# Performance work log

Hardware: AMD Instinct MI355X
Metric: run time of the kernel (lower is better)

## Reference

```python
import jax, jax.numpy as jnp
import numpy as np
import math

B, S, D = 1, 4096, 2048
H, KVH, HD = 32, 8, 64
W = 512            # sliding window size (== block size)
THETA = 10000.0
EPS = 1e-5
INTER = 5632
PRE_SCALE = 1.0 / math.sqrt(2.0)


def setup_inputs() -> dict:
    key = jax.random.key(0)
    ks = jax.random.split(key, 8)
    def w(k, shape, fan_in):
        return jax.random.normal(k, shape, jnp.float32) * (fan_in ** -0.5)
    return {
        "hidden_states": jax.random.normal(ks[0], (B, S, D), jnp.float32),
        "mixer_norm_w": jnp.ones((D,), jnp.float32),
        "wq": w(ks[1], (D, H * HD), D),
        "wk": w(ks[2], (D, KVH * HD), D),
        "wv": w(ks[3], (D, KVH * HD), D),
        "wo": w(ks[4], (H * HD, D), H * HD),
        "mlp_norm_w": jnp.ones((D,), jnp.float32),
        "w_gate": w(ks[5], (D, 2 * INTER), D),
        "w_down": w(ks[6], (INTER, D), INTER),
    }


def rmsnorm(x, w, eps=EPS):
    return x * jax.lax.rsqrt(jnp.mean(x * x, axis=-1, keepdims=True) + eps) * w


def rope(x):
    # x: [B, S, h, HD]; rotate-half RoPE
    half = HD // 2
    inv_freq = 1.0 / (THETA ** (jnp.arange(0, HD, 2, dtype=jnp.float32) / HD))
    freqs = jnp.arange(S, dtype=jnp.float32)[:, None] * inv_freq[None, :]  # [S, half]
    cos = jnp.cos(freqs)[None, :, None, :]
    sin = jnp.sin(freqs)[None, :, None, :]
    x1, x2 = x[..., :half], x[..., half:]
    return jnp.concatenate([x1 * cos - x2 * sin, x2 * cos + x1 * sin], axis=-1)


def sliding_attention(x, wq, wk, wv, wo):
    # x already pre-scaled; returns attn output (pre /pre_scale)
    q = (x @ wq).reshape(B, S, H, HD)
    k = (x @ wk).reshape(B, S, KVH, HD)
    v = (x @ wv).reshape(B, S, KVH, HD)
    q, k = rope(q), rope(k)
    rep = H // KVH
    k = jnp.repeat(k, rep, axis=2)  # [B,S,H,HD]
    v = jnp.repeat(v, rep, axis=2)
    nb = S // W
    qb = q.reshape(B, nb, W, H, HD)
    kb = k.reshape(B, nb, W, H, HD)
    vb = v.reshape(B, nb, W, H, HD)
    zeros = jnp.zeros((B, 1, W, H, HD), q.dtype)
    kw = jnp.concatenate([jnp.concatenate([zeros, kb[:, :-1]], axis=1), kb], axis=2)  # [B,nb,2W,H,HD]
    vw = jnp.concatenate([jnp.concatenate([zeros, vb[:, :-1]], axis=1), vb], axis=2)
    # local mask [nb, W, 2W]
    blk = jnp.arange(nb)[:, None, None]
    q_pos = blk * W + jnp.arange(W)[None, :, None]
    k_pos = blk * W - W + jnp.arange(2 * W)[None, None, :]
    mask = (k_pos >= 0) & (k_pos <= q_pos) & (q_pos - k_pos < W)
    scores = jnp.einsum("bnqhd,bnkhd->bhnqk", qb, kw) * (HD ** -0.5)
    scores = jnp.where(mask[None, None], scores, jnp.finfo(scores.dtype).min)
    p = jax.nn.softmax(scores, axis=-1)
    out = jnp.einsum("bhnqk,bnkhd->bnqhd", p, vw).reshape(B, S, H * HD)
    return out @ wo


def reference(hidden_states, mixer_norm_w, wq, wk, wv, wo, mlp_norm_w, w_gate, w_down):
    residual = hidden_states
    x = rmsnorm(hidden_states, mixer_norm_w)
    attn_out = sliding_attention(x * PRE_SCALE, wq, wk, wv, wo) / PRE_SCALE
    h = residual + attn_out
    xn = rmsnorm(h, mlp_norm_w)
    gv = xn @ w_gate
    gate, y = gv[..., :INTER], gv[..., INTER:]
    mlp_out = (jax.nn.silu(gate) * y) @ w_down
    return h + mlp_out
```

## Files before the change

kernel.cpp:

```cpp
#include <hip/hip_runtime.h>
#include <stdint.h>

typedef __attribute__((ext_vector_type(8))) short s16x8;
typedef __attribute__((ext_vector_type(4))) float f32x4;

#define GLD_LDS16(gp, lp) __builtin_amdgcn_global_load_lds( \
    (__attribute__((address_space(1))) void*)(void*)(gp), \
    (__attribute__((address_space(3))) void*)(lp), 16, 0, 0)

__device__ __forceinline__ float b2f(unsigned short s) {
    unsigned int u = ((unsigned int)s) << 16;
    return __builtin_bit_cast(float, u);
}
__device__ __forceinline__ unsigned short f2b(float f) {
    unsigned int u = __builtin_bit_cast(unsigned int, f);
    u = (u + 0x7FFFu + ((u >> 16) & 1u)) >> 16;
    return (unsigned short)u;
}
__device__ __forceinline__ f32x4 mfma16(s16x8 a, s16x8 b, f32x4 c) {
    return __builtin_amdgcn_mfma_f32_16x16x32_bf16(a, b, c, 0, 0, 0);
}
template <int N> __device__ __forceinline__ void waitvm() {
    if constexpr (N == 3) asm volatile("s_waitcnt vmcnt(3)" ::: "memory");
    else if constexpr (N == 4) asm volatile("s_waitcnt vmcnt(4)" ::: "memory");
    else if constexpr (N == 6) asm volatile("s_waitcnt vmcnt(6)" ::: "memory");
}

__global__ __launch_bounds__(256) void rmsnorm_bf16(
    const float* __restrict__ x, const float* __restrict__ wgt,
    unsigned short* __restrict__ out)
{
    const int row = blockIdx.x;
    const int t = threadIdx.x;
    const float* xr = x + (size_t)row * 2048;
    float4 a = *(const float4*)(xr + t * 8);
    float4 b = *(const float4*)(xr + t * 8 + 4);
    float ss = a.x*a.x + a.y*a.y + a.z*a.z + a.w*a.w
             + b.x*b.x + b.y*b.y + b.z*b.z + b.w*b.w;
    #pragma unroll
    for (int d = 1; d < 64; d <<= 1) ss += __shfl_xor(ss, d);
    __shared__ float red[4];
    if ((t & 63) == 0) red[t >> 6] = ss;
    __syncthreads();
    float tot = red[0] + red[1] + red[2] + red[3];
    float inv = rsqrtf(tot * (1.0f / 2048.0f) + 1e-5f);
    float vals[8] = {a.x, a.y, a.z, a.w, b.x, b.y, b.z, b.w};
    const float* wr_ = wgt + t * 8;
    s16x8 ov;
    #pragma unroll
    for (int j = 0; j < 8; ++j) ov[j] = (short)f2b(vals[j] * inv * wr_[j]);
    *(s16x8*)(out + (size_t)row * 2048 + t * 8) = ov;
}

__global__ __launch_bounds__(256) void transpose_to_bf16(
    const float* __restrict__ in, unsigned short* __restrict__ out, int K, int N)
{
    __shared__ float tile[32][33];
    int n0 = blockIdx.x * 32, k0 = blockIdx.y * 32;
    int r = threadIdx.x >> 5, c = threadIdx.x & 31;
    #pragma unroll
    for (int i = 0; i < 4; ++i)
        tile[r + i * 8][c] = in[(size_t)(k0 + r + i * 8) * N + n0 + c];
    __syncthreads();
    #pragma unroll
    for (int i = 0; i < 4; ++i)
        out[(size_t)(n0 + r + i * 8) * K + k0 + c] = f2b(tile[c][r + i * 8]);
}

template <int BN, int EPI>
__global__ __launch_bounds__(512, 2) void gemmq(
    const unsigned short* __restrict__ A,
    const unsigned short* __restrict__ B,
    void* __restrict__ Cv,
    const float* __restrict__ ADD,
    int N, int K)
{
    constexpr int WN  = BN / 4;
    constexpr int HN  = WN / 2;
    constexpr int NJQ = WN / 32;
    constexpr int NBU = BN / 64;
    constexpr int ABUF = 256 * 64;
    constexpr int BBUF = BN * 64;
    constexpr int W_P0 = 4;
    constexpr int W_P1 = (BN == 256) ? 6 : 4;
    constexpr int W_P2 = (BN == 256) ? 4 : 3;
    __shared__ __align__(16) unsigned short As[2 * ABUF];
    __shared__ __align__(16) unsigned short Bs[2 * BBUF];

    const int t = threadIdx.x;
    const int l = t & 63, w = t >> 6;
    const int l15 = l & 15, lg = l >> 4;
    const int wr = w >> 2, wc = w & 3;
    const int x7 = l15 & 7;
    const int cc0 = ((lg) ^ x7) << 3;
    const int cc1 = ((4 | lg) ^ x7) << 3;

    const int nwg = (int)gridDim.x;
    const int orig = (int)blockIdx.x;
    const int q8 = nwg >> 3, r8 = nwg & 7;
    const int xcd = orig & 7, lid = orig >> 3;
    const int wg = (xcd < r8 ? xcd * (q8 + 1) : r8 * (q8 + 1) + (xcd - r8) * q8) + lid;
    const int m0 = (wg & 15) * 256;
    const int n0 = (wg >> 4) * BN;

    const int tr = t >> 3;
    const int scol = ((t & 7) ^ (tr & 7)) << 3;
    const unsigned short* pA[4];
    #pragma unroll
    for (int u = 0; u < 4; ++u) {
        const int lrow = u * 64 + tr;
        const int g = ((lrow >> 6) & 1) * 128 + (lrow >> 7) * 64 + (lrow & 63);
        pA[u] = A + (size_t)(m0 + g) * K + scol;
    }
    const unsigned short* pB[NBU];
    #pragma unroll
    for (int u = 0; u < NBU; ++u) {
        const int lrow = u * 64 + tr;
        const int h = lrow / (BN / 2), rem = lrow % (BN / 2);
        const int g = (rem / HN) * WN + h * HN + (rem % HN);
        pB[u] = B + (size_t)(n0 + g) * K + scol;
    }

    f32x4 acc[2][2][4][NJQ] = {};
    s16x8 aF[4][2];
    s16x8 bF[2][NJQ][2];

    const int NT = K / 64;

    GLD_LDS16(pA[0], &As[0 * 4096 + t * 8]);
    GLD_LDS16(pA[1], &As[1 * 4096 + t * 8]);
    #pragma unroll
    for (int u = 0; u < NBU; ++u) GLD_LDS16(pB[u], &Bs[u * 4096 + t * 8]);
    GLD_LDS16(pA[2], &As[2 * 4096 + t * 8]);
    GLD_LDS16(pA[3], &As[3 * 4096 + t * 8]);
    waitvm<W_P2>();
    __builtin_amdgcn_s_barrier();

    for (int kt = 0; kt < NT; ++kt) {
        const int rb  = (kt & 1) ? ABUF : 0;
        const int rbB = (kt & 1) ? BBUF : 0;
        const int wb  = ABUF - rb;
        const int wbB = BBUF - rbB;
        const int knext = (kt + 1 < NT ? kt + 1 : kt) * 64;

        #pragma unroll
        for (int i = 0; i < 4; ++i) {
            const int lr = wr * 64 + i * 16 + l15;
            aF[i][0] = *(const s16x8*)&As[rb + lr * 64 + cc0];
            aF[i][1] = *(const s16x8*)&As[rb + lr * 64 + cc1];
        }
        #pragma unroll
        for (int j = 0; j < NJQ; ++j) {
            const int lr = wc * HN + j * 16 + l15;
            bF[0][j][0] = *(const s16x8*)&Bs[rbB + lr * 64 + cc0];
            bF[0][j][1] = *(const s16x8*)&Bs[rbB + lr * 64 + cc1];
        }
        GLD_LDS16(pA[0] + knext, &As[wb + 0 * 4096 + t * 8]);
        GLD_LDS16(pA[1] + knext, &As[wb + 1 * 4096 + t * 8]);
        __builtin_amdgcn_s_barrier();
        __builtin_amdgcn_s_setprio(1);
        #pragma unroll
        for (int kk = 0; kk < 2; ++kk)
            #pragma unroll
            for (int i = 0; i < 4; ++i)
                #pragma unroll
                for (int j = 0; j < NJQ; ++j)
                    acc[0][0][i][j] = mfma16(aF[i][kk], bF[0][j][kk], acc[0][0][i][j]);
        __builtin_amdgcn_s_setprio(0);
        waitvm<W_P0>();
        __builtin_amdgcn_s_barrier();

        #pragma unroll
        for (int j = 0; j < NJQ; ++j) {
            const int lr = (BN / 2) + wc * HN + j * 16 + l15;
            bF[1][j][0] = *(const s16x8*)&Bs[rbB + lr * 64 + cc0];
            bF[1][j][1] = *(const s16x8*)&Bs[rbB + lr * 64 + cc1];
        }
        #pragma unroll
        for (int u = 0; u < NBU; ++u)
            GLD_LDS16(pB[u] + knext, &Bs[wbB + u * 4096 + t * 8]);
        __builtin_amdgcn_s_barrier();
        __builtin_amdgcn_s_setprio(1);
        #pragma unroll
        for (int kk = 0; kk < 2; ++kk)
            #pragma unroll
            for (int i = 0; i < 4; ++i)
                #pragma unroll
                for (int j = 0; j < NJQ; ++j)
                    acc[0][1][i][j] = mfma16(aF[i][kk], bF[1][j][kk], acc[0][1][i][j]);
        __builtin_amdgcn_s_setprio(0);
        waitvm<W_P1>();
        __builtin_amdgcn_s_barrier();

        #pragma unroll
        for (int i = 0; i < 4; ++i) {
            const int lr = 128 + wr * 64 + i * 16 + l15;
            aF[i][0] = *(const s16x8*)&As[rb + lr * 64 + cc0];
            aF[i][1] = *(const s16x8*)&As[rb + lr * 64 + cc1];
        }
        GLD_LDS16(pA[2] + knext, &As[wb + 2 * 4096 + t * 8]);
        GLD_LDS16(pA[3] + knext, &As[wb + 3 * 4096 + t * 8]);
        __builtin_amdgcn_s_barrier();
        __builtin_amdgcn_s_setprio(1);
        #pragma unroll
        for (int kk = 0; kk < 2; ++kk)
            #pragma unroll
            for (int i = 0; i < 4; ++i)
                #pragma unroll
                for (int j = 0; j < NJQ; ++j)
                    acc[1][0][i][j] = mfma16(aF[i][kk], bF[0][j][kk], acc[1][0][i][j]);
        #pragma unroll
        for (int kk = 0; kk < 2; ++kk)
            #pragma unroll
            for (int i = 0; i < 4; ++i)
                #pragma unroll
                for (int j = 0; j < NJQ; ++j)
                    acc[1][1][i][j] = mfma16(aF[i][kk], bF[1][j][kk], acc[1][1][i][j]);
        __builtin_amdgcn_s_setprio(0);
        waitvm<W_P2>();
        __builtin_amdgcn_s_barrier();
    }

    #pragma unroll
    for (int qm = 0; qm < 2; ++qm)
        #pragma unroll
        for (int i = 0; i < 4; ++i)
            #pragma unroll
            for (int r = 0; r < 4; ++r) {
                const int row = m0 + wr * 128 + qm * 64 + i * 16 + lg * 4 + r;
                const size_t rbase = (size_t)row * N;
                #pragma unroll
                for (int qn = 0; qn < 2; ++qn)
                    #pragma unroll
                    for (int j = 0; j < NJQ; ++j) {
                        const int col = n0 + wc * WN + qn * HN + j * 16 + l15;
                        float v = acc[qm][qn][i][j][r];
                        if constexpr (EPI == 0) {
                            ((unsigned short*)Cv)[rbase + col] = f2b(v);
                        } else {
                            ((float*)Cv)[rbase + col] = v + ADD[rbase + col];
                        }
                    }
            }
}

__global__ __launch_bounds__(512, 2) void gemm_glu(
    const unsigned short* __restrict__ A,
    const unsigned short* __restrict__ Bg,
    const unsigned short* __restrict__ By,
    unsigned short* __restrict__ act,
    int N, int K)
{
    constexpr int ABUF = 256 * 64, BBUF = 128 * 64;
    __shared__ __align__(16) unsigned short As[2 * ABUF];
    __shared__ __align__(16) unsigned short Bgs[2 * BBUF];
    __shared__ __align__(16) unsigned short Bys[2 * BBUF];

    const int t = threadIdx.x;
    const int l = t & 63, w = t >> 6;
    const int l15 = l & 15, lg = l >> 4;
    const int wr = w >> 2, wc = w & 3;
    const int x7 = l15 & 7;
    const int cc0 = ((lg) ^ x7) << 3;
    const int cc1 = ((4 | lg) ^ x7) << 3;

    const int nwg = (int)gridDim.x;
    const int orig = (int)blockIdx.x;
    const int q8 = nwg >> 3;
    const int xcd = orig & 7, lid = orig >> 3;
    const int wg = xcd * q8 + lid;
    const int m0 = (wg & 15) * 256;
    const int n0 = (wg >> 4) * 128;

    const int tr = t >> 3;
    const int scol = ((t & 7) ^ (tr & 7)) << 3;
    const unsigned short* pA[4];
    #pragma unroll
    for (int u = 0; u < 4; ++u) {
        const int lrow = u * 64 + tr;
        const int g = ((lrow >> 6) & 1) * 128 + (lrow >> 7) * 64 + (lrow & 63);
        pA[u] = A + (size_t)(m0 + g) * K + scol;
    }
    const unsigned short *pG[2], *pY[2];
    #pragma unroll
    for (int u = 0; u < 2; ++u) {
        const int g = (tr >> 4) * 32 + u * 16 + (tr & 15);
        pG[u] = Bg + (size_t)(n0 + g) * K + scol;
        pY[u] = By + (size_t)(n0 + g) * K + scol;
    }

    f32x4 accG[2][2][4] = {};
    f32x4 accY[2][2][4] = {};
    s16x8 aF[4][2];
    s16x8 gF[2][2], yF[2][2];

    const int NT = K / 64;

    GLD_LDS16(pA[0], &As[0 * 4096 + t * 8]);
    GLD_LDS16(pA[1], &As[1 * 4096 + t * 8]);
    GLD_LDS16(pG[0], &Bgs[0 * 4096 + t * 8]);
    GLD_LDS16(pY[0], &Bys[0 * 4096 + t * 8]);
    GLD_LDS16(pG[1], &Bgs[1 * 4096 + t * 8]);
    GLD_LDS16(pY[1], &Bys[1 * 4096 + t * 8]);
    GLD_LDS16(pA[2], &As[2 * 4096 + t * 8]);
    GLD_LDS16(pA[3], &As[3 * 4096 + t * 8]);
    waitvm<4>();
    __builtin_amdgcn_s_barrier();

    for (int kt = 0; kt < NT; ++kt) {
        const int rb  = (kt & 1) ? ABUF : 0;
        const int rbB = (kt & 1) ? BBUF : 0;
        const int wb  = ABUF - rb;
        const int wbB = BBUF - rbB;
        const int knext = (kt + 1 < NT ? kt + 1 : kt) * 64;

        #pragma unroll
        for (int i = 0; i < 4; ++i) {
            const int lr = wr * 64 + i * 16 + l15;
            aF[i][0] = *(const s16x8*)&As[rb + lr * 64 + cc0];
            aF[i][1] = *(const s16x8*)&As[rb + lr * 64 + cc1];
        }
        {
            const int lr = wc * 16 + l15;
            gF[0][0] = *(const s16x8*)&Bgs[rbB + lr * 64 + cc0];
            gF[0][1] = *(const s16x8*)&Bgs[rbB + lr * 64 + cc1];
            yF[0][0] = *(const s16x8*)&Bys[rbB + lr * 64 + cc0];
            yF[0][1] = *(const s16x8*)&Bys[rbB + lr * 64 + cc1];
        }
        GLD_LDS16(pA[0] + knext, &As[wb + 0 * 4096 + t * 8]);
        GLD_LDS16(pA[1] + knext, &As[wb + 1 * 4096 + t * 8]);
        __builtin_amdgcn_s_barrier();
        __builtin_amdgcn_s_setprio(1);
        #pragma unroll
        for (int kk = 0; kk < 2; ++kk)
            #pragma unroll
            for (int i = 0; i < 4; ++i) {
                accG[0][0][i] = mfma16(aF[i][kk], gF[0][kk], accG[0][0][i]);
                accY[0][0][i] = mfma16(aF[i][kk], yF[0][kk], accY[0][0][i]);
            }
        __builtin_amdgcn_s_setprio(0);
        waitvm<4>();
        __builtin_amdgcn_s_barrier();

        {
            const int lr = 64 + wc * 16 + l15;
            gF[1][0] = *(const s16x8*)&Bgs[rbB + lr * 64 + cc0];
            gF[1][1] = *(const s16x8*)&Bgs[rbB + lr * 64 + cc1];
            yF[1][0] = *(const s16x8*)&Bys[rbB + lr * 64 + cc0];
            yF[1][1] = *(const s16x8*)&Bys[rbB + lr * 64 + cc1];
        }
        GLD_LDS16(pG[0] + knext, &Bgs[wbB + 0 * 4096 + t * 8]);
        GLD_LDS16(pY[0] + knext, &Bys[wbB + 0 * 4096 + t * 8]);
        GLD_LDS16(pG[1] + knext, &Bgs[wbB + 1 * 4096 + t * 8]);
        GLD_LDS16(pY[1] + knext, &Bys[wbB + 1 * 4096 + t * 8]);
        __builtin_amdgcn_s_barrier();
        __builtin_amdgcn_s_setprio(1);
        #pragma unroll
        for (int kk = 0; kk < 2; ++kk)
            #pragma unroll
            for (int i = 0; i < 4; ++i) {
                accG[0][1][i] = mfma16(aF[i][kk], gF[1][kk], accG[0][1][i]);
                accY[0][1][i] = mfma16(aF[i][kk], yF[1][kk], accY[0][1][i]);
            }
        __builtin_amdgcn_s_setprio(0);
        waitvm<6>();
        __builtin_amdgcn_s_barrier();

        #pragma unroll
        for (int i = 0; i < 4; ++i) {
            const int lr = 128 + wr * 64 + i * 16 + l15;
            aF[i][0] = *(const s16x8*)&As[rb + lr * 64 + cc0];
            aF[i][1] = *(const s16x8*)&As[rb + lr * 64 + cc1];
        }
        GLD_LDS16(pA[2] + knext, &As[wb + 2 * 4096 + t * 8]);
        GLD_LDS16(pA[3] + knext, &As[wb + 3 * 4096 + t * 8]);
        __builtin_amdgcn_s_barrier();
        __builtin_amdgcn_s_setprio(1);
        #pragma unroll
        for (int kk = 0; kk < 2; ++kk)
            #pragma unroll
            for (int i = 0; i < 4; ++i) {
                accG[1][0][i] = mfma16(aF[i][kk], gF[0][kk], accG[1][0][i]);
                accY[1][0][i] = mfma16(aF[i][kk], yF[0][kk], accY[1][0][i]);
            }
        #pragma unroll
        for (int kk = 0; kk < 2; ++kk)
            #pragma unroll
            for (int i = 0; i < 4; ++i) {
                accG[1][1][i] = mfma16(aF[i][kk], gF[1][kk], accG[1][1][i]);
                accY[1][1][i] = mfma16(aF[i][kk], yF[1][kk], accY[1][1][i]);
            }
        __builtin_amdgcn_s_setprio(0);
        waitvm<4>();
        __builtin_amdgcn_s_barrier();
    }

    #pragma unroll
    for (int qm = 0; qm < 2; ++qm)
        #pragma unroll
        for (int i = 0; i < 4; ++i)
            #pragma unroll
            for (int r = 0; r < 4; ++r) {
                const int row = m0 + wr * 128 + qm * 64 + i * 16 + lg * 4 + r;
                const size_t rbase = (size_t)row * N;
                #pragma unroll
                for (int qn = 0; qn < 2; ++qn) {
                    const int col = n0 + wc * 32 + qn * 16 + l15;
                    float g = accG[qm][qn][i][r];
                    float y = accY[qm][qn][i][r];
                    float sg = g / (1.0f + expf(-g));
                    act[rbase + col] = f2b(sg * y);
                }
            }
}

__global__ void rope_tab_k(float2* __restrict__ tab) {
    int i = blockIdx.x * 256 + threadIdx.x;
    if (i >= 4096 * 32) return;
    int s = i >> 5, d = i & 31;
    float inv = exp2f(-(float)d * (13.287712379549449f / 32.0f));
    float fr = (float)s * inv;
    float sv, cv;
    sincosf(fr, &sv, &cv);
    tab[i] = make_float2(cv, sv);
}

__global__ void rope_apply_k(unsigned short* __restrict__ qkv, const float2* __restrict__ tab) {
    int i = blockIdx.x * 256 + threadIdx.x;
    if (i >= 4096 * 40 * 4) return;
    int dg = i & 3;
    int rest = i >> 2;
    int head = rest % 40;
    int s = rest / 40;
    int off = head < 32 ? head * 64 : 2048 + (head - 32) * 64;
    unsigned short* p = qkv + (size_t)s * 3072 + off + dg * 8;
    s16x8 x1 = *(const s16x8*)p;
    s16x8 x2 = *(const s16x8*)(p + 32);
    const float2* tb = tab + s * 32 + dg * 8;
    s16x8 o1, o2;
    #pragma unroll
    for (int j = 0; j < 8; ++j) {
        float2 cs = tb[j];
        float a = b2f((unsigned short)x1[j]);
        float b = b2f((unsigned short)x2[j]);
        o1[j] = (short)f2b(a * cs.x - b * cs.y);
        o2[j] = (short)f2b(b * cs.x + a * cs.y);
    }
    *(s16x8*)p = o1;
    *(s16x8*)(p + 32) = o2;
}

__global__ __launch_bounds__(256) void attn_swa(
    const unsigned short* __restrict__ qkv,
    unsigned short* __restrict__ out)
{
    constexpr int LDQ = 3072;
    const int qb = blockIdx.x;
    const int h = blockIdx.y;
    const int kvh = h >> 2;
    const int q0 = qb * 64;
    const int t = threadIdx.x, l = t & 63, w = t >> 6;
    const int l15 = l & 15, lg = l >> 4;

    __shared__ unsigned short Kl[64 * 64];
    __shared__ unsigned short Vt[64 * 72];
    __shared__ unsigned short Pl[4 * 16 * 72];

    s16x8 qf[2];
    {
        const unsigned short* qp = qkv + (size_t)(q0 + w * 16 + l15) * LDQ + h * 64 + lg * 8;
        qf[0] = *(const s16x8*)(qp);
        qf[1] = *(const s16x8*)(qp + 32);
    }
    float m_run[4] = {-1e30f, -1e30f, -1e30f, -1e30f};
    float l_run[4] = {0.f, 0.f, 0.f, 0.f};
    f32x4 o[4] = {};

    const float SC = 0.0625f * 1.4426950408889634f;
    const int kt_lo = qb >= 8 ? qb - 8 : 0;

    for (int kt = kt_lo; kt <= qb; ++kt) {
        const int ks = kt * 64;
        __syncthreads();
        {
            const unsigned short* kg = qkv + (size_t)(ks + (t >> 3)) * LDQ + 2048 + kvh * 64 + (t & 7) * 8;
            GLD_LDS16(kg, Kl + t * 8);
            GLD_LDS16(kg + (size_t)32 * LDQ, Kl + t * 8 + 2048);
        }
        {
            const unsigned short* vg = qkv + (size_t)(ks + l) * LDQ + 2560 + kvh * 64 + w * 16;
            s16x8 v0 = *(const s16x8*)vg;
            s16x8 v1 = *(const s16x8*)(vg + 8);
            #pragma unroll
            for (int j = 0; j < 8; ++j) Vt[(w * 16 + j) * 72 + l] = (unsigned short)v0[j];
            #pragma unroll
            for (int j = 0; j < 8; ++j) Vt[(w * 16 + 8 + j) * 72 + l] = (unsigned short)v1[j];
        }
        __syncthreads();

        f32x4 sf[4] = {};
        #pragma unroll
        for (int kf = 0; kf < 4; ++kf) {
            #pragma unroll
            for (int kk = 0; kk < 2; ++kk) {
                s16x8 kb = *(const s16x8*)(Kl + (kf * 16 + l15) * 64 + kk * 32 + lg * 8);
                sf[kf] = mfma16(qf[kk], kb, sf[kf]);
            }
        }

        float tmax[4];
        #pragma unroll
        for (int r = 0; r < 4; ++r) {
            int qrow = q0 + w * 16 + lg * 4 + r;
            float mx = -1e30f;
            #pragma unroll
            for (int kf = 0; kf < 4; ++kf) {
                int key = ks + kf * 16 + l15;
                bool valid = (key <= qrow) && (qrow - key < 512);
                if (valid) mx = fmaxf(mx, sf[kf][r]);
            }
            #pragma unroll
            for (int d2 = 1; d2 < 16; d2 <<= 1) mx = fmaxf(mx, __shfl_xor(mx, d2));
            tmax[r] = mx;
        }

        float alpha[4], rsum[4];
        #pragma unroll
        for (int r = 0; r < 4; ++r) {
            float mnew = fmaxf(m_run[r], tmax[r]);
            alpha[r] = exp2f((m_run[r] - mnew) * SC);
            m_run[r] = mnew;
            rsum[r] = 0.f;
        }

        unsigned short* Pw = Pl + w * (16 * 72);
        #pragma unroll
        for (int kf = 0; kf < 4; ++kf) {
            #pragma unroll
            for (int r = 0; r < 4; ++r) {
                int qrow = q0 + w * 16 + lg * 4 + r;
                int key = ks + kf * 16 + l15;
                bool valid = (key <= qrow) && (qrow - key < 512);
                float p = valid ? exp2f((sf[kf][r] - m_run[r]) * SC) : 0.f;
                rsum[r] += p;
                Pw[(lg * 4 + r) * 72 + kf * 16 + l15] = f2b(p);
            }
        }
        #pragma unroll
        for (int r = 0; r < 4; ++r) {
            #pragma unroll
            for (int d2 = 1; d2 < 16; d2 <<= 1) rsum[r] += __shfl_xor(rsum[r], d2);
            l_run[r] = l_run[r] * alpha[r] + rsum[r];
        }
        #pragma unroll
        for (int hf = 0; hf < 4; ++hf)
            #pragma unroll
            for (int r = 0; r < 4; ++r) o[hf][r] *= alpha[r];

        asm volatile("s_waitcnt lgkmcnt(0)" ::: "memory");
        __builtin_amdgcn_sched_barrier(0);

        #pragma unroll
        for (int kk2 = 0; kk2 < 2; ++kk2) {
            s16x8 pa = *(const s16x8*)(Pw + l15 * 72 + kk2 * 32 + lg * 8);
            #pragma unroll
            for (int hf = 0; hf < 4; ++hf) {
                s16x8 vb = *(const s16x8*)(Vt + (hf * 16 + l15) * 72 + kk2 * 32 + lg * 8);
                o[hf] = mfma16(pa, vb, o[hf]);
            }
        }
    }

    #pragma unroll
    for (int r = 0; r < 4; ++r) {
        int qrow = q0 + w * 16 + lg * 4 + r;
        float invl = 1.0f / l_run[r];
        unsigned short* orow = out + (size_t)qrow * 2048 + h * 64;
        #pragma unroll
        for (int hf = 0; hf < 4; ++hf)
            orow[hf * 16 + l15] = f2b(o[hf][r] * invl);
    }
}

extern "C" void kernel_launch(void* const* d_in, const int* in_sizes, int n_in,
                              void* d_out, int out_size, void* d_ws, size_t ws_size,
                              hipStream_t stream)
{
    const float* hidden = (const float*)d_in[0];
    const float* w_mix  = (const float*)d_in[1];
    const float* wq     = (const float*)d_in[2];
    const float* wk     = (const float*)d_in[3];
    const float* wv     = (const float*)d_in[4];
    const float* wo     = (const float*)d_in[5];
    const float* w_mlp  = (const float*)d_in[6];
    const float* wg     = (const float*)d_in[7];
    const float* wd     = (const float*)d_in[8];
    float* out = (float*)d_out;

    char* ws = (char*)d_ws;
    size_t off = 0;
    auto alloc = [&](size_t bytes) {
        char* p = ws + off;
        off += (bytes + 255) & ~(size_t)255;
        return p;
    };
    unsigned short* Wt   = (unsigned short*)alloc((size_t)11264 * 2048 * 2);
    unsigned short* xn   = (unsigned short*)alloc((size_t)4096 * 2048 * 2);
    unsigned short* qkv  = (unsigned short*)alloc((size_t)4096 * 3072 * 2);
    float2*         rtab = (float2*)alloc((size_t)4096 * 32 * 8);
    unsigned short* attn = (unsigned short*)alloc((size_t)4096 * 2048 * 2);
    float*          hbuf = (float*)alloc((size_t)4096 * 2048 * 4);
    unsigned short* act  = (unsigned short*)alloc((size_t)4096 * 5632 * 2);

    rmsnorm_bf16<<<4096, 256, 0, stream>>>(hidden, w_mix, xn);

    transpose_to_bf16<<<dim3(64, 64), 256, 0, stream>>>(wq, Wt, 2048, 2048);
    transpose_to_bf16<<<dim3(16, 64), 256, 0, stream>>>(wk, Wt + (size_t)2048 * 2048, 2048, 512);
    transpose_to_bf16<<<dim3(16, 64), 256, 0, stream>>>(wv, Wt + (size_t)2560 * 2048, 2048, 512);

    gemmq<256, 0><<<192, 512, 0, stream>>>(xn, Wt, qkv, nullptr, 3072, 2048);

    rope_tab_k<<<(4096 * 32 + 255) / 256, 256, 0, stream>>>(rtab);
    rope_apply_k<<<(4096 * 40 * 4 + 255) / 256, 256, 0, stream>>>(qkv, rtab);

    attn_swa<<<dim3(64, 32), 256, 0, stream>>>(qkv, attn);

    transpose_to_bf16<<<dim3(64, 64), 256, 0, stream>>>(wo, Wt, 2048, 2048);
    gemmq<128, 1><<<256, 512, 0, stream>>>(attn, Wt, hbuf, hidden, 2048, 2048);

    rmsnorm_bf16<<<4096, 256, 0, stream>>>(hbuf, w_mlp, xn);

    transpose_to_bf16<<<dim3(352, 64), 256, 0, stream>>>(wg, Wt, 2048, 11264);
    gemm_glu<<<704, 512, 0, stream>>>(xn, Wt, Wt + (size_t)5632 * 2048, act, 5632, 2048);

    transpose_to_bf16<<<dim3(64, 176), 256, 0, stream>>>(wd, Wt, 5632, 2048);
    gemmq<128, 1><<<256, 512, 0, stream>>>(act, Wt, out, hbuf, 2048, 5632);
}
```

Before: 551.8 us.

## Spread GEMM global-to-LDS loads across four phases and widen weight transpose tiles

The GEMM main loops (gemmq and gemm_glu) now split the B-tile prefetches across two compute phases and move the second A-half prefetch into a new fourth phase with an extra barrier, retuning the vmcnt waits to match. The goal is to issue fewer outstanding loads per phase so memory traffic overlaps MFMA work more evenly, at the cost of one more barrier per k-step. Separately, the weight transpose kernel now uses 64x64 tiles with float4 loads and 16-byte bf16 stores, cutting the number of memory transactions for the per-call weight conversions.

```diff
diff --git a/kernel.cpp b/kernel.cpp
--- a/kernel.cpp
+++ b/kernel.cpp
@@ -23,7 +23,6 @@
 template <int N> __device__ __forceinline__ void waitvm() {
     if constexpr (N == 3) asm volatile("s_waitcnt vmcnt(3)" ::: "memory");
     else if constexpr (N == 4) asm volatile("s_waitcnt vmcnt(4)" ::: "memory");
-    else if constexpr (N == 6) asm volatile("s_waitcnt vmcnt(6)" ::: "memory");
 }
 
 __global__ __launch_bounds__(256) void rmsnorm_bf16(
@@ -55,16 +54,27 @@
 __global__ __launch_bounds__(256) void transpose_to_bf16(
     const float* __restrict__ in, unsigned short* __restrict__ out, int K, int N)
 {
-    __shared__ float tile[32][33];
-    int n0 = blockIdx.x * 32, k0 = blockIdx.y * 32;
-    int r = threadIdx.x >> 5, c = threadIdx.x & 31;
-    #pragma unroll
-    for (int i = 0; i < 4; ++i)
-        tile[r + i * 8][c] = in[(size_t)(k0 + r + i * 8) * N + n0 + c];
+    __shared__ float tile[64][65];
+    const int n0 = blockIdx.x * 64, k0 = blockIdx.y * 64;
+    const int t = threadIdx.x;
+    const int kr = t >> 4, nc = (t & 15) * 4;
+    #pragma unroll
+    for (int i = 0; i < 4; ++i) {
+        float4 v = *(const float4*)(in + (size_t)(k0 + kr + i * 16) * N + n0 + nc);
+        tile[nc + 0][kr + i * 16] = v.x;
+        tile[nc + 1][kr + i * 16] = v.y;
+        tile[nc + 2][kr + i * 16] = v.z;
+        tile[nc + 3][kr + i * 16] = v.w;
+    }
     __syncthreads();
-    #pragma unroll
-    for (int i = 0; i < 4; ++i)
-        out[(size_t)(n0 + r + i * 8) * K + k0 + c] = f2b(tile[c][r + i * 8]);
+    const int nr = t >> 3, kc = (t & 7) * 8;
+    #pragma unroll
+    for (int p = 0; p < 2; ++p) {
+        s16x8 o;
+        #pragma unroll
+        for (int j = 0; j < 8; ++j) o[j] = (short)f2b(tile[nr + p * 32][kc + j]);
+        *(s16x8*)(out + (size_t)(n0 + nr + p * 32) * K + k0 + kc) = o;
+    }
 }
 
 template <int BN, int EPI>
@@ -81,9 +91,9 @@
     constexpr int NBU = BN / 64;
     constexpr int ABUF = 256 * 64;
     constexpr int BBUF = BN * 64;
-    constexpr int W_P0 = 4;
-    constexpr int W_P1 = (BN == 256) ? 6 : 4;
-    constexpr int W_P2 = (BN == 256) ? 4 : 3;
+    constexpr int W1   = 4;
+    constexpr int W2   = (BN == 256) ? 4 : 3;
+    constexpr int WEND = (BN == 256) ? 4 : 3;
     __shared__ __align__(16) unsigned short As[2 * ABUF];
     __shared__ __align__(16) unsigned short Bs[2 * BBUF];
 
@@ -133,7 +143,7 @@
     for (int u = 0; u < NBU; ++u) GLD_LDS16(pB[u], &Bs[u * 4096 + t * 8]);
     GLD_LDS16(pA[2], &As[2 * 4096 + t * 8]);
     GLD_LDS16(pA[3], &As[3 * 4096 + t * 8]);
-    waitvm<W_P2>();
+    waitvm<WEND>();
     __builtin_amdgcn_s_barrier();
 
     for (int kt = 0; kt < NT; ++kt) {
@@ -167,7 +177,7 @@
                 for (int j = 0; j < NJQ; ++j)
                     acc[0][0][i][j] = mfma16(aF[i][kk], bF[0][j][kk], acc[0][0][i][j]);
         __builtin_amdgcn_s_setprio(0);
-        waitvm<W_P0>();
+        waitvm<W1>();
         __builtin_amdgcn_s_barrier();
 
         #pragma unroll
@@ -177,7 +187,7 @@
             bF[1][j][1] = *(const s16x8*)&Bs[rbB + lr * 64 + cc1];
         }
         #pragma unroll
-        for (int u = 0; u < NBU; ++u)
+        for (int u = 0; u < NBU / 2; ++u)
             GLD_LDS16(pB[u] + knext, &Bs[wbB + u * 4096 + t * 8]);
         __builtin_amdgcn_s_barrier();
         __builtin_amdgcn_s_setprio(1);
@@ -189,7 +199,7 @@
                 for (int j = 0; j < NJQ; ++j)
                     acc[0][1][i][j] = mfma16(aF[i][kk], bF[1][j][kk], acc[0][1][i][j]);
         __builtin_amdgcn_s_setprio(0);
-        waitvm<W_P1>();
+        waitvm<W2>();
         __builtin_amdgcn_s_barrier();
 
         #pragma unroll
@@ -198,8 +208,9 @@
             aF[i][0] = *(const s16x8*)&As[rb + lr * 64 + cc0];
             aF[i][1] = *(const s16x8*)&As[rb + lr * 64 + cc1];
         }
-        GLD_LDS16(pA[2] + knext, &As[wb + 2 * 4096 + t * 8]);
-        GLD_LDS16(pA[3] + knext, &As[wb + 3 * 4096 + t * 8]);
+        #pragma unroll
+        for (int u = NBU / 2; u < NBU; ++u)
+            GLD_LDS16(pB[u] + knext, &Bs[wbB + u * 4096 + t * 8]);
         __builtin_amdgcn_s_barrier();
         __builtin_amdgcn_s_setprio(1);
         #pragma unroll
@@ -209,6 +220,13 @@
                 #pragma unroll
                 for (int j = 0; j < NJQ; ++j)
                     acc[1][0][i][j] = mfma16(aF[i][kk], bF[0][j][kk], acc[1][0][i][j]);
+        __builtin_amdgcn_s_setprio(0);
+        __builtin_amdgcn_s_barrier();
+
+        GLD_LDS16(pA[2] + knext, &As[wb + 2 * 4096 + t * 8]);
+        GLD_LDS16(pA[3] + knext, &As[wb + 3 * 4096 + t * 8]);
+        __builtin_amdgcn_s_barrier();
+        __builtin_amdgcn_s_setprio(1);
         #pragma unroll
         for (int kk = 0; kk < 2; ++kk)
             #pragma unroll
@@ -217,7 +235,7 @@
                 for (int j = 0; j < NJQ; ++j)
                     acc[1][1][i][j] = mfma16(aF[i][kk], bF[1][j][kk], acc[1][1][i][j]);
         __builtin_amdgcn_s_setprio(0);
-        waitvm<W_P2>();
+        waitvm<WEND>();
         __builtin_amdgcn_s_barrier();
     }
 
@@ -351,8 +369,6 @@
         }
         GLD_LDS16(pG[0] + knext, &Bgs[wbB + 0 * 4096 + t * 8]);
         GLD_LDS16(pY[0] + knext, &Bys[wbB + 0 * 4096 + t * 8]);
-        GLD_LDS16(pG[1] + knext, &Bgs[wbB + 1 * 4096 + t * 8]);
-        GLD_LDS16(pY[1] + knext, &Bys[wbB + 1 * 4096 + t * 8]);
         __builtin_amdgcn_s_barrier();
         __builtin_amdgcn_s_setprio(1);
         #pragma unroll
@@ -363,7 +379,7 @@
                 accY[0][1][i] = mfma16(aF[i][kk], yF[1][kk], accY[0][1][i]);
             }
         __builtin_amdgcn_s_setprio(0);
-        waitvm<6>();
+        waitvm<4>();
         __builtin_amdgcn_s_barrier();
 
         #pragma unroll
@@ -372,8 +388,8 @@
             aF[i][0] = *(const s16x8*)&As[rb + lr * 64 + cc0];
             aF[i][1] = *(const s16x8*)&As[rb + lr * 64 + cc1];
         }
-        GLD_LDS16(pA[2] + knext, &As[wb + 2 * 4096 + t * 8]);
-        GLD_LDS16(pA[3] + knext, &As[wb + 3 * 4096 + t * 8]);
+        GLD_LDS16(pG[1] + knext, &Bgs[wbB + 1 * 4096 + t * 8]);
+        GLD_LDS16(pY[1] + knext, &Bys[wbB + 1 * 4096 + t * 8]);
         __builtin_amdgcn_s_barrier();
         __builtin_amdgcn_s_setprio(1);
         #pragma unroll
@@ -383,6 +399,13 @@
                 accG[1][0][i] = mfma16(aF[i][kk], gF[0][kk], accG[1][0][i]);
                 accY[1][0][i] = mfma16(aF[i][kk], yF[0][kk], accY[1][0][i]);
             }
+        __builtin_amdgcn_s_setprio(0);
+        __builtin_amdgcn_s_barrier();
+
+        GLD_LDS16(pA[2] + knext, &As[wb + 2 * 4096 + t * 8]);
+        GLD_LDS16(pA[3] + knext, &As[wb + 3 * 4096 + t * 8]);
+        __builtin_amdgcn_s_barrier();
+        __builtin_amdgcn_s_setprio(1);
         #pragma unroll
         for (int kk = 0; kk < 2; ++kk)
             #pragma unroll
@@ -614,9 +637,9 @@
 
     rmsnorm_bf16<<<4096, 256, 0, stream>>>(hidden, w_mix, xn);
 
-    transpose_to_bf16<<<dim3(64, 64), 256, 0, stream>>>(wq, Wt, 2048, 2048);
-    transpose_to_bf16<<<dim3(16, 64), 256, 0, stream>>>(wk, Wt + (size_t)2048 * 2048, 2048, 512);
-    transpose_to_bf16<<<dim3(16, 64), 256, 0, stream>>>(wv, Wt + (size_t)2560 * 2048, 2048, 512);
+    transpose_to_bf16<<<dim3(32, 32), 256, 0, stream>>>(wq, Wt, 2048, 2048);
+    transpose_to_bf16<<<dim3(8, 32), 256, 0, stream>>>(wk, Wt + (size_t)2048 * 2048, 2048, 512);
+    transpose_to_bf16<<<dim3(8, 32), 256, 0, stream>>>(wv, Wt + (size_t)2560 * 2048, 2048, 512);
 
     gemmq<256, 0><<<192, 512, 0, stream>>>(xn, Wt, qkv, nullptr, 3072, 2048);
 
@@ -625,14 +648,14 @@
 
     attn_swa<<<dim3(64, 32), 256, 0, stream>>>(qkv, attn);
 
-    transpose_to_bf16<<<dim3(64, 64), 256, 0, stream>>>(wo, Wt, 2048, 2048);
+    transpose_to_bf16<<<dim3(32, 32), 256, 0, stream>>>(wo, Wt, 2048, 2048);
     gemmq<128, 1><<<256, 512, 0, stream>>>(attn, Wt, hbuf, hidden, 2048, 2048);
 
     rmsnorm_bf16<<<4096, 256, 0, stream>>>(hbuf, w_mlp, xn);
 
-    transpose_to_bf16<<<dim3(352, 64), 256, 0, stream>>>(wg, Wt, 2048, 11264);
+    transpose_to_bf16<<<dim3(176, 32), 256, 0, stream>>>(wg, Wt, 2048, 11264);
     gemm_glu<<<704, 512, 0, stream>>>(xn, Wt, Wt + (size_t)5632 * 2048, act, 5632, 2048);
 
-    transpose_to_bf16<<<dim3(64, 176), 256, 0, stream>>>(wd, Wt, 5632, 2048);
+    transpose_to_bf16<<<dim3(32, 88), 256, 0, stream>>>(wd, Wt, 5632, 2048);
     gemmq<128, 1><<<256, 512, 0, stream>>>(act, Wt, out, hbuf, 2048, 5632);
 }
```

Result: no change. 550.4 us (-0.3%).
